# Optimization experiments

Measured on AMD Instinct MI355X. Metric: run time of the kernel, lower is better.

## Reference

```python
import jax, jax.numpy as jnp
import numpy as np

D_MODEL, D_STATE, D_CONV, EXPAND, HEADDIM, NGROUPS, CHUNK = 1024, 64, 4, 2, 64, 1, 64
D_INNER = EXPAND * D_MODEL          # 2048
NHEADS = D_INNER // HEADDIM         # 32
CONV_DIM = D_INNER + 2 * NGROUPS * D_STATE  # 2176
D_IN_PROJ = 2 * D_INNER + 2 * NGROUPS * D_STATE + NHEADS  # 4256
EPS = 1e-5


def segsum(x):
    """x: (..., T) -> (..., T, T) with out[i,j]=sum_{j<k<=i} x[k], -inf above diag."""
    T = x.shape[-1]
    i = jnp.arange(T)[:, None]
    j = jnp.arange(T)[None, :]
    xr = jnp.where(i > j, x[..., :, None], 0.0)   # keep x[...,i] at (i,j) when i>j
    s = jnp.cumsum(xr, axis=-2)
    return jnp.where(i >= j, s, -jnp.inf)


def setup_inputs() -> dict:
    key = jax.random.key(0)
    ks = jax.random.split(key, 10)
    B, L = 4, 4096
    u = jax.random.normal(ks[0], (B, L, D_MODEL), dtype=jnp.float32)
    in_proj_w = jax.random.normal(ks[1], (D_IN_PROJ, D_MODEL), dtype=jnp.float32) * (D_MODEL ** -0.5)
    conv_w = jax.random.normal(ks[2], (CONV_DIM, D_CONV), dtype=jnp.float32) * (D_CONV ** -0.5)
    conv_b = jax.random.normal(ks[3], (CONV_DIM,), dtype=jnp.float32) * 0.02
    init_states = jax.random.normal(ks[4], (NHEADS, HEADDIM, D_STATE), dtype=jnp.float32) * 0.02
    # dt_bias = inv softplus of dt sampled log-uniform in [1e-3, 1e-1]
    dt = jnp.exp(jax.random.uniform(ks[5], (NHEADS,)) * (np.log(0.1) - np.log(0.001)) + np.log(0.001))
    dt = jnp.clip(dt, 1e-4, None)
    dt_bias = dt + jnp.log(-jnp.expm1(-dt))
    A_log = jnp.log(jax.random.uniform(ks[6], (NHEADS,), minval=1.0, maxval=16.0))
    D = jnp.ones((NHEADS,), dtype=jnp.float32)
    norm_w = jnp.ones((D_INNER,), dtype=jnp.float32)
    out_proj_w = jax.random.normal(ks[7], (D_MODEL, D_INNER), dtype=jnp.float32) * (D_INNER ** -0.5)
    return {"u": u, "in_proj_w": in_proj_w, "conv_w": conv_w, "conv_b": conv_b,
            "init_states": init_states, "dt_bias": dt_bias, "A_log": A_log, "D": D,
            "norm_w": norm_w, "out_proj_w": out_proj_w}


def _forward(u, in_proj_w, conv_w, conv_b, init_states, dt_bias, A_log, D, norm_w, out_proj_w):
    b, L, _ = u.shape
    zxbcdt = jnp.einsum('bld,ed->ble', u, in_proj_w)
    z = zxbcdt[..., :D_INNER]
    xBC = zxbcdt[..., D_INNER:D_INNER + CONV_DIM]
    dt = jax.nn.softplus(zxbcdt[..., D_INNER + CONV_DIM:] + dt_bias)  # (b,L,h)
    # causal depthwise conv1d (padding=K-1, truncated to L) + SiLU
    xp = jnp.pad(xBC, ((0, 0), (D_CONV - 1, 0), (0, 0)))
    xBC = sum(xp[:, k:k + L, :] * conv_w[:, k] for k in range(D_CONV)) + conv_b
    xBC = jax.nn.silu(xBC)
    x = xBC[..., :D_INNER].reshape(b, L, NHEADS, HEADDIM)
    Bm = xBC[..., D_INNER:D_INNER + NGROUPS * D_STATE].reshape(b, L, NGROUPS, D_STATE)
    Cm = xBC[..., D_INNER + NGROUPS * D_STATE:].reshape(b, L, NGROUPS, D_STATE)
    A = -jnp.exp(A_log)  # (h,)
    # broadcast groups to heads (torch einsum broadcasts size-1 group dim)
    Bm = jnp.repeat(Bm, NHEADS // NGROUPS, axis=2)
    Cm = jnp.repeat(Cm, NHEADS // NGROUPS, axis=2)
    X = x * dt[..., None]          # (b,L,h,p)
    Adt = A * dt                   # (b,L,h)
    c = L // CHUNK
    Xc = X.reshape(b, c, CHUNK, NHEADS, HEADDIM)
    Bc = Bm.reshape(b, c, CHUNK, NHEADS, D_STATE)
    Cc = Cm.reshape(b, c, CHUNK, NHEADS, D_STATE)
    Ac = Adt.reshape(b, c, CHUNK, NHEADS).transpose(0, 3, 1, 2)  # (b,h,c,l)
    A_cumsum = jnp.cumsum(Ac, axis=-1)
    Lmat = jnp.exp(segsum(Ac))  # (b,h,c,l,l)
    Y_diag = jnp.einsum('bclhn,bcshn,bhcls,bcshp->bclhp', Cc, Bc, Lmat, Xc)
    decay_states = jnp.exp(A_cumsum[..., -1:] - A_cumsum)  # (b,h,c,l)
    states = jnp.einsum('bclhn,bhcl,bclhp->bchpn', Bc, decay_states, Xc)
    init = jnp.broadcast_to(init_states, (b,) + init_states.shape)[:, None]  # (b,1,h,p,n)
    states = jnp.concatenate([init, states], axis=1)  # (b,c+1,h,p,n)
    decay_chunk = jnp.exp(segsum(jnp.pad(A_cumsum[..., -1], ((0, 0), (0, 0), (1, 0)))))
    new_states = jnp.einsum('bhzc,bchpn->bzhpn', decay_chunk, states)
    states = new_states[:, :-1]
    state_decay_out = jnp.exp(A_cumsum)
    Y_off = jnp.einsum('bclhn,bchpn,bhcl->bclhp', Cc, states, state_decay_out)
    Y = (Y_diag + Y_off).reshape(b, L, NHEADS, HEADDIM) + x * D[:, None]
    y = Y.reshape(b, L, D_INNER)
    # gated RMSNorm (gate before norm)
    y = y * jax.nn.silu(z)
    y = y * jax.lax.rsqrt(jnp.mean(y * y, axis=-1, keepdims=True) + EPS) * norm_w
    return jnp.einsum('bld,ed->ble', y, out_proj_w)


def reference(u, in_proj_w, conv_w, conv_b, init_states, dt_bias, A_log, D, norm_w, out_proj_w):
    return _forward(u, in_proj_w, conv_w, conv_b, init_states, dt_bias, A_log, D, norm_w, out_proj_w)
```

## Files before the change

kernel.cpp:

```cpp
#include <hip/hip_runtime.h>
#include <math.h>

#define BATCH  4
#define LSEQ   4096
#define DMODEL 1024
#define DINNER 2048
#define NH     32
#define HD     64
#define DSTATE 64
#define CONVD  2176
#define NPROJ  4352
#define ZROW   4224
#define NCHUNK 64

typedef __attribute__((ext_vector_type(8))) short bf16x8;
typedef __attribute__((ext_vector_type(4))) float f32x4;

__device__ __forceinline__ float sigm(float x){ return 1.f/(1.f+expf(-x)); }

__device__ __forceinline__ unsigned short f2bf(float x){
    unsigned u = __float_as_uint(x);
    unsigned r = (u + 0x7fffu + ((u>>16)&1u)) >> 16;
    return (unsigned short)r;
}
__device__ __forceinline__ float bf2f(unsigned short h){
    return __uint_as_float(((unsigned)h)<<16);
}

__device__ __forceinline__ void gl2lds16(const unsigned short* g, short* l){
    __builtin_amdgcn_global_load_lds(
        (const __attribute__((address_space(1))) unsigned int*)g,
        (__attribute__((address_space(3))) unsigned int*)l, 16, 0, 0);
}

__global__ __launch_bounds__(256)
void f32_to_bf16(const float* __restrict__ in, unsigned short* __restrict__ o, size_t n)
{
    size_t i = ((size_t)blockIdx.x*256 + threadIdx.x)*8;
    if (i >= n) return;
    float4 a = *(const float4*)(in + i);
    float4 b = *(const float4*)(in + i + 4);
    uint4 v;
    v.x = (unsigned)f2bf(a.x) | ((unsigned)f2bf(a.y)<<16);
    v.y = (unsigned)f2bf(a.z) | ((unsigned)f2bf(a.w)<<16);
    v.z = (unsigned)f2bf(b.x) | ((unsigned)f2bf(b.y)<<16);
    v.w = (unsigned)f2bf(b.z) | ((unsigned)f2bf(b.w)<<16);
    *(uint4*)(o + i) = v;
}

template<int EPI>
__global__ __launch_bounds__(256)
void gemm_mfma(const unsigned short* __restrict__ A,
               const unsigned short* __restrict__ B,
               int K, int lda, int ldc, int ntiles, int Mrows,
               float* __restrict__ Cf,
               unsigned short* __restrict__ zxbc,
               float* __restrict__ dtout,
               const float* __restrict__ dt_bias,
               unsigned short* __restrict__ halo)
{
    __shared__ short As[128*64];
    __shared__ short Bs[128*64];
    const int tid  = threadIdx.x;
    const int wave = tid >> 6;
    const int lane = tid & 63;

    const int GM  = 16;
    const int pid = blockIdx.x;
    const int gsz = GM * ntiles;
    const int grp = pid / gsz;
    const int rem = pid - grp*gsz;
    const int bm  = (grp*GM + (rem & (GM-1))) * 128;
    const int bn  = (rem / GM) * 128;

    const int wr = (wave >> 1) * 64;
    const int wc = (wave & 1) * 64;
    const int quad = lane >> 4;
    const int l15  = lane & 15;

    f32x4 acc[4][4];
    #pragma unroll
    for (int i=0;i<4;i++)
        #pragma unroll
        for (int j=0;j<4;j++)
            acc[i][j] = (f32x4){0.f,0.f,0.f,0.f};

    const int srow8 = lane >> 3;
    const int scolx = ((lane & 7) ^ srow8) * 8;
    const int rsw   = (l15 & 7);

    for (int k0 = 0; k0 < K; k0 += 64){
        #pragma unroll
        for (int s=0; s<4; s++){
            int t = wave*4 + s;
            int r = t*8 + srow8;
            gl2lds16(A + (size_t)(bm + r)*lda + k0 + scolx, &As[t*512]);
            gl2lds16(B + (size_t)(bn + r)*K   + k0 + scolx, &Bs[t*512]);
        }
        __syncthreads();
        #pragma unroll
        for (int ks=0; ks<2; ks++){
            bf16x8 af[4], bg[4];
            #pragma unroll
            for (int i=0;i<4;i++)
                af[i] = *(const bf16x8*)&As[(wr + i*16 + l15)*64 + (((ks*4 + quad) ^ rsw)<<3)];
            #pragma unroll
            for (int j=0;j<4;j++)
                bg[j] = *(const bf16x8*)&Bs[(wc + j*16 + l15)*64 + (((ks*4 + quad) ^ rsw)<<3)];
            #pragma unroll
            for (int i=0;i<4;i++)
                #pragma unroll
                for (int j=0;j<4;j++)
                    acc[i][j] = __builtin_amdgcn_mfma_f32_16x16x32_bf16(af[i], bg[j], acc[i][j], 0,0,0);
        }
        __syncthreads();
    }

    if (EPI == 0){
        #pragma unroll
        for (int i=0;i<4;i++)
            #pragma unroll
            for (int j=0;j<4;j++){
                int col = bn + wc + j*16 + l15;
                #pragma unroll
                for (int r=0;r<4;r++){
                    int row = bm + wr + i*16 + quad*4 + r;
                    Cf[(size_t)row*ldc + col] = acc[i][j][r];
                }
            }
    } else {
        if (bn < DINNER){
            #pragma unroll
            for (int i=0;i<4;i++)
                #pragma unroll
                for (int r=0;r<4;r++){
                    int row = bm + wr + i*16 + quad*4 + r;
                    #pragma unroll
                    for (int j=0;j<4;j++){
                        int col = bn + wc + j*16 + l15;
                        zxbc[(size_t)row*ZROW + col] = f2bf(acc[i][j][r]);
                    }
                }
        } else if (bn < DINNER + CONVD){
            #pragma unroll
            for (int i=0;i<4;i++)
                #pragma unroll
                for (int r=0;r<4;r++){
                    int row = bm + wr + i*16 + quad*4 + r;
                    int rel = row & 63;
                    int seg = (row >> 6) + 1;
                    #pragma unroll
                    for (int j=0;j<4;j++){
                        int col = bn + wc + j*16 + l15;
                        unsigned short v = f2bf(acc[i][j][r]);
                        zxbc[(size_t)row*ZROW + col] = v;
                        if (rel >= 61 && seg*64 < Mrows)
                            halo[((size_t)(seg*3 + (rel-61)))*CONVD + (col - DINNER)] = v;
                    }
                }
        } else if (wc == 0){
            #pragma unroll
            for (int j=0;j<2;j++){
                int h = j*16 + l15;
                #pragma unroll
                for (int i=0;i<4;i++)
                    #pragma unroll
                    for (int r=0;r<4;r++){
                        int row = bm + wr + i*16 + quad*4 + r;
                        float t = acc[i][j][r] + dt_bias[h];
                        dtout[(size_t)row*NH + h] = (t > 20.f) ? t : log1pf(expf(t));
                    }
            }
        }
    }
}

__global__ __launch_bounds__(256)
void conv_inplace(unsigned short* __restrict__ zxbc,
                  const unsigned short* __restrict__ halo,
                  const float* __restrict__ conv_w, const float* __restrict__ conv_b)
{
    int c = blockIdx.x*256 + threadIdx.x;
    if (c >= CONVD) return;
    int seg = blockIdx.y;
    const float w0=conv_w[c*4+0], w1=conv_w[c*4+1], w2=conv_w[c*4+2], w3=conv_w[c*4+3];
    const float bias = conv_b[c];
    float x0=0.f, x1=0.f, x2=0.f;
    if ((seg & 63) != 0){
        const unsigned short* hp = halo + (size_t)(seg*3)*CONVD + c;
        x0 = bf2f(hp[0]); x1 = bf2f(hp[CONVD]); x2 = bf2f(hp[2*CONVD]);
    }
    unsigned short* p = zxbc + (size_t)(seg*64)*ZROW + DINNER + c;
    for (int i=0;i<64;i++){
        float x3 = bf2f(*p);
        float v = fmaf(w0,x0,fmaf(w1,x1,fmaf(w2,x2,fmaf(w3,x3,bias))));
        *p = f2bf(v * sigm(v));
        x0=x1; x1=x2; x2=x3; p += ZROW;
    }
}

__global__ __launch_bounds__(256)
void states_intra(const unsigned short* __restrict__ zxbc,
                  const float* __restrict__ dtbuf,
                  const float* __restrict__ A_log,
                  unsigned short* __restrict__ locst,
                  float* __restrict__ acsbuf,
                  float* __restrict__ csumbuf)
{
    const int h = blockIdx.x, c = blockIdx.y;
    __shared__ unsigned short XT[64*72];
    __shared__ unsigned short BT[64*72];
    __shared__ float dt_sh[64], acs_sh[64], w_sh[64];
    const int tid = threadIdx.x;
    const size_t row0 = (size_t)(c*64)*ZROW;

    if (tid < 64) dt_sh[tid] = dtbuf[(size_t)(c*64+tid)*NH + h];
    __syncthreads();
    if (tid == 0){
        float Ah = -expf(A_log[h]); float s = 0.f;
        for (int l=0;l<64;l++){ s = fmaf(Ah, dt_sh[l], s); acs_sh[l] = s; }
    }
    __syncthreads();
    const float a63 = acs_sh[63];
    if (tid < 64){
        float a = acs_sh[tid];
        acsbuf[((size_t)c*NH + h)*64 + tid] = a;
        w_sh[tid] = expf(a63 - a) * dt_sh[tid];
    }
    if (tid == 0) csumbuf[(size_t)c*NH + h] = a63;
    __syncthreads();

    {
        const int l  = tid >> 2;
        const int f4 = tid & 3;
        const unsigned short* xr = zxbc + row0 + (size_t)l*ZROW;
        const float w = w_sh[l];
        #pragma unroll
        for (int q=0;q<4;q++){
            int col = f4*4 + q*16;
            uint2 xv = *(const uint2*)(xr + DINNER + h*HD + col);
            uint2 bv = *(const uint2*)(xr + DINNER + DINNER + col);
            XT[(col+0)*72 + l] = (unsigned short)(xv.x & 0xffff);
            XT[(col+1)*72 + l] = (unsigned short)(xv.x >> 16);
            XT[(col+2)*72 + l] = (unsigned short)(xv.y & 0xffff);
            XT[(col+3)*72 + l] = (unsigned short)(xv.y >> 16);
            BT[(col+0)*72 + l] = f2bf(bf2f((unsigned short)(bv.x & 0xffff))*w);
            BT[(col+1)*72 + l] = f2bf(bf2f((unsigned short)(bv.x >> 16))*w);
            BT[(col+2)*72 + l] = f2bf(bf2f((unsigned short)(bv.y & 0xffff))*w);
            BT[(col+3)*72 + l] = f2bf(bf2f((unsigned short)(bv.y >> 16))*w);
        }
    }
    __syncthreads();

    const int wave = tid >> 6, lane = tid & 63;
    const int quad = lane >> 4, l15 = lane & 15;
    f32x4 acc[4];
    #pragma unroll
    for (int j=0;j<4;j++) acc[j] = (f32x4){0.f,0.f,0.f,0.f};
    #pragma unroll
    for (int ks=0;ks<2;ks++){
        bf16x8 af = *(const bf16x8*)&XT[(wave*16 + l15)*72 + ks*32 + quad*8];
        #pragma unroll
        for (int j=0;j<4;j++){
            bf16x8 bf = *(const bf16x8*)&BT[(j*16 + l15)*72 + ks*32 + quad*8];
            acc[j] = __builtin_amdgcn_mfma_f32_16x16x32_bf16(af, bf, acc[j], 0,0,0);
        }
    }
    const size_t sbase = ((size_t)c*NH + h)*4096;
    #pragma unroll
    for (int j=0;j<4;j++)
        #pragma unroll
        for (int r=0;r<4;r++){
            int p = wave*16 + quad*4 + r;
            int n = j*16 + l15;
            locst[sbase + (size_t)p*64 + n] = f2bf(acc[j][r]);
        }
}

__global__ __launch_bounds__(256)
void chunk_scan(unsigned short* __restrict__ states,
                const float* __restrict__ csumbuf,
                const float* __restrict__ init_states)
{
    const int h = blockIdx.x, half = blockIdx.y, b = blockIdx.z;
    __shared__ float cs_sh[64];
    const int tid = threadIdx.x;
    if (tid < 64) cs_sh[tid] = csumbuf[(size_t)(b*64 + tid)*NH + h];
    __syncthreads();
    const int e0 = half*2048 + tid*8;
    float S[8];
    {
        const float4* ip = (const float4*)(init_states + (size_t)h*4096 + e0);
        float4 v0 = ip[0], v1 = ip[1];
        S[0]=v0.x; S[1]=v0.y; S[2]=v0.z; S[3]=v0.w;
        S[4]=v1.x; S[5]=v1.y; S[6]=v1.z; S[7]=v1.w;
    }
    for (int zg=0; zg<8; zg++){
        uint4 L[8];
        #pragma unroll
        for (int k=0;k<8;k++)
            L[k] = *(const uint4*)(states + ((size_t)(b*64 + zg*8+k)*NH + h)*4096 + e0);
        #pragma unroll
        for (int k=0;k<8;k++){
            int z = zg*8 + k;
            float dec = expf(cs_sh[z]);
            uint4 o;
            o.x = (unsigned)f2bf(S[0]) | ((unsigned)f2bf(S[1])<<16);
            o.y = (unsigned)f2bf(S[2]) | ((unsigned)f2bf(S[3])<<16);
            o.z = (unsigned)f2bf(S[4]) | ((unsigned)f2bf(S[5])<<16);
            o.w = (unsigned)f2bf(S[6]) | ((unsigned)f2bf(S[7])<<16);
            *(uint4*)(states + ((size_t)(b*64 + z)*NH + h)*4096 + e0) = o;
            unsigned a[4] = {L[k].x, L[k].y, L[k].z, L[k].w};
            #pragma unroll
            for (int q=0;q<4;q++){
                float lo = bf2f((unsigned short)(a[q]&0xffff));
                float hi = bf2f((unsigned short)(a[q]>>16));
                S[q*2+0] = fmaf(dec, S[q*2+0], lo);
                S[q*2+1] = fmaf(dec, S[q*2+1], hi);
            }
        }
    }
}

__global__ __launch_bounds__(256)
void y_fused(unsigned short* __restrict__ zxbc,
             const float* __restrict__ dtbuf,
             const unsigned short* __restrict__ entst,
             const float* __restrict__ acsbuf,
             const float* __restrict__ Dvec)
{
    const int h = blockIdx.x, c = blockIdx.y;
    __shared__ unsigned short Cr[64*72];
    __shared__ unsigned short Ce[64*72];
    __shared__ unsigned short Bm[64*72];
    __shared__ unsigned short XT[64*72];
    __shared__ unsigned short Sv[64*72];
    __shared__ float acs_sh[64], dt_sh[64], ea_sh[64];
    const int tid = threadIdx.x;
    const size_t row0 = (size_t)(c*64)*ZROW;
    const size_t sbase = ((size_t)c*NH + h)*4096;

    if (tid < 64){
        float a = acsbuf[((size_t)c*NH + h)*64 + tid];
        acs_sh[tid] = a;
        ea_sh[tid]  = expf(a);
        dt_sh[tid]  = dtbuf[(size_t)(c*64 + tid)*NH + h];
    }
    __syncthreads();

    {
        const int l  = tid >> 2;
        const int f4 = tid & 3;
        const unsigned short* xr = zxbc + row0 + (size_t)l*ZROW;
        const float el = ea_sh[l];
        #pragma unroll
        for (int q=0;q<4;q++){
            int col = f4*4 + q*16;
            uint2 cv = *(const uint2*)(xr + DINNER + DINNER + DSTATE + col);
            uint2 bv = *(const uint2*)(xr + DINNER + DINNER + col);
            uint2 xv = *(const uint2*)(xr + DINNER + h*HD + col);
            *(uint2*)&Cr[l*72 + col] = cv;
            *(uint2*)&Bm[l*72 + col] = bv;
            unsigned short* ce = &Ce[l*72 + col];
            ce[0] = f2bf(bf2f((unsigned short)(cv.x & 0xffff))*el);
            ce[1] = f2bf(bf2f((unsigned short)(cv.x >> 16))*el);
            ce[2] = f2bf(bf2f((unsigned short)(cv.y & 0xffff))*el);
            ce[3] = f2bf(bf2f((unsigned short)(cv.y >> 16))*el);
            XT[(col+0)*72 + l] = (unsigned short)(xv.x & 0xffff);
            XT[(col+1)*72 + l] = (unsigned short)(xv.x >> 16);
            XT[(col+2)*72 + l] = (unsigned short)(xv.y & 0xffff);
            XT[(col+3)*72 + l] = (unsigned short)(xv.y >> 16);
            *(uint2*)&Sv[l*72 + col] = *(const uint2*)(entst + sbase + (size_t)l*64 + col);
        }
    }
    __syncthreads();

    const int wave = tid >> 6, lane = tid & 63;
    const int quad = lane >> 4, l15 = lane & 15;

    f32x4 g[4];
    #pragma unroll
    for (int j=0;j<4;j++) g[j] = (f32x4){0.f,0.f,0.f,0.f};
    #pragma unroll
    for (int ks=0;ks<2;ks++){
        bf16x8 af = *(const bf16x8*)&Cr[(wave*16 + l15)*72 + ks*32 + quad*8];
        #pragma unroll
        for (int j=0;j<4;j++){
            bf16x8 bf = *(const bf16x8*)&Bm[(j*16 + l15)*72 + ks*32 + quad*8];
            g[j] = __builtin_amdgcn_mfma_f32_16x16x32_bf16(af, bf, g[j], 0,0,0);
        }
    }
    __syncthreads();

    const float Dh = Dvec[h];
    #pragma unroll
    for (int j=0;j<4;j++)
        #pragma unroll
        for (int r=0;r<4;r++){
            int l = wave*16 + quad*4 + r;
            int s = j*16 + l15;
            float v = (s <= l) ? g[j][r]*expf(acs_sh[l]-acs_sh[s])*dt_sh[s] : 0.f;
            if (s == l) v += Dh;
            Bm[l*72 + s] = f2bf(v);
        }
    __syncthreads();

    f32x4 y[4];
    #pragma unroll
    for (int j=0;j<4;j++) y[j] = (f32x4){0.f,0.f,0.f,0.f};
    #pragma unroll
    for (int ks=0;ks<2;ks++){
        bf16x8 a1 = *(const bf16x8*)&Bm[(wave*16 + l15)*72 + ks*32 + quad*8];
        bf16x8 a2 = *(const bf16x8*)&Ce[(wave*16 + l15)*72 + ks*32 + quad*8];
        #pragma unroll
        for (int j=0;j<4;j++){
            bf16x8 b1 = *(const bf16x8*)&XT[(j*16 + l15)*72 + ks*32 + quad*8];
            bf16x8 b2 = *(const bf16x8*)&Sv[(j*16 + l15)*72 + ks*32 + quad*8];
            y[j] = __builtin_amdgcn_mfma_f32_16x16x32_bf16(a1, b1, y[j], 0,0,0);
            y[j] = __builtin_amdgcn_mfma_f32_16x16x32_bf16(a2, b2, y[j], 0,0,0);
        }
    }

    #pragma unroll
    for (int j=0;j<4;j++)
        #pragma unroll
        for (int r=0;r<4;r++){
            int l = wave*16 + quad*4 + r;
            int p = j*16 + l15;
            zxbc[row0 + (size_t)l*ZROW + DINNER + h*HD + p] = f2bf(y[j][r]);
        }
}

__global__ __launch_bounds__(256)
void gate_norm(unsigned short* __restrict__ zxbc, const float* __restrict__ norm_w)
{
    const int m = blockIdx.x;
    const int tid = threadIdx.x;
    unsigned short* row = zxbc + (size_t)m*ZROW;
    uint4 zv = *(const uint4*)(row + tid*8);
    uint4 yv = *(const uint4*)(row + DINNER + tid*8);
    unsigned zz[4] = {zv.x, zv.y, zv.z, zv.w};
    unsigned yy[4] = {yv.x, yv.y, yv.z, yv.w};
    float g[8];
    float acc = 0.f;
    #pragma unroll
    for (int q=0;q<4;q++){
        float zl = bf2f((unsigned short)(zz[q]&0xffff));
        float zh = bf2f((unsigned short)(zz[q]>>16));
        float yl = bf2f((unsigned short)(yy[q]&0xffff));
        float yh = bf2f((unsigned short)(yy[q]>>16));
        g[q*2+0] = yl * zl * sigm(zl);
        g[q*2+1] = yh * zh * sigm(zh);
        acc += g[q*2]*g[q*2] + g[q*2+1]*g[q*2+1];
    }
    #pragma unroll
    for (int o=32;o>0;o>>=1) acc += __shfl_down(acc, o, 64);
    __shared__ float red[4];
    if ((tid & 63)==0) red[tid>>6] = acc;
    __syncthreads();
    float tot = red[0]+red[1]+red[2]+red[3];
    float scale = rsqrtf(tot * (1.f/2048.f) + 1e-5f);
    const float* nw = norm_w + tid*8;
    float4 w0 = *(const float4*)nw;
    float4 w1 = *(const float4*)(nw+4);
    float Wv[8] = {w0.x,w0.y,w0.z,w0.w,w1.x,w1.y,w1.z,w1.w};
    uint4 ov;
    unsigned ow[4];
    #pragma unroll
    for (int q=0;q<4;q++){
        unsigned short lo = f2bf(g[q*2+0]*scale*Wv[q*2+0]);
        unsigned short hi = f2bf(g[q*2+1]*scale*Wv[q*2+1]);
        ow[q] = (unsigned)lo | ((unsigned)hi<<16);
    }
    ov.x=ow[0]; ov.y=ow[1]; ov.z=ow[2]; ov.w=ow[3];
    *(uint4*)(row + tid*8) = ov;
}

extern "C" void kernel_launch(void* const* d_in, const int* in_sizes, int n_in,
                              void* d_out, int out_size, void* d_ws, size_t ws_size,
                              hipStream_t stream) {
    const float* u           = (const float*)d_in[0];
    const float* in_proj_w   = (const float*)d_in[1];
    const float* conv_w      = (const float*)d_in[2];
    const float* conv_b      = (const float*)d_in[3];
    const float* init_states = (const float*)d_in[4];
    const float* dt_bias     = (const float*)d_in[5];
    const float* A_log       = (const float*)d_in[6];
    const float* Dv          = (const float*)d_in[7];
    const float* norm_w      = (const float*)d_in[8];
    const float* out_proj_w  = (const float*)d_in[9];
    float* out = (float*)d_out;
    char* wsb = (char*)d_ws;

    const size_t BIG_BYTES = 226197504;
    const bool big = (ws_size >= BIG_BYTES);
    const int nb = big ? BATCH : 1;
    const size_t Mrows = (size_t)nb * LSEQ;

    size_t off = 0;
    unsigned short* zxbc    = (unsigned short*)(wsb + off); off += Mrows*ZROW*2;
    unsigned short* statesz = (unsigned short*)(wsb + off);
    unsigned short* ubf     = statesz;
    off += Mrows/64 * NH*HD*DSTATE*2;
    unsigned short* wibf    = (unsigned short*)(wsb + off); off += (size_t)NPROJ*DMODEL*2;
    unsigned short* woutbf  = (unsigned short*)(wsb + off); off += (size_t)DMODEL*DINNER*2;
    float*          dtbuf   = (float*)(wsb + off);   off += Mrows*NH*4;
    float*          acsbuf  = (float*)(wsb + off);   off += Mrows/64 * NH*64*4;
    float*          csumbuf = (float*)(wsb + off);   off += Mrows/64 * NH*4;
    unsigned short* halo    = (unsigned short*)(wsb + off); off += Mrows/64 * 3*CONVD*2;

    f32_to_bf16<<<dim3((4256*1024/8 + 255)/256), 256, 0, stream>>>(
        in_proj_w, wibf, (size_t)4256*1024);
    f32_to_bf16<<<dim3(1024*2048/8/256), 256, 0, stream>>>(
        out_proj_w, woutbf, (size_t)1024*2048);

    const int npass = big ? 1 : BATCH;
    for (int b=0; b<npass; b++){
        const float* ub   = u   + (size_t)b*LSEQ*DMODEL;
        float*       outb = out + (size_t)b*LSEQ*DMODEL;
        const int mt = (int)(Mrows/128);

        f32_to_bf16<<<dim3(Mrows*DMODEL/8/256), 256, 0, stream>>>(
            ub, ubf, Mrows*DMODEL);
        gemm_mfma<1><<<dim3((NPROJ/128) * mt), 256, 0, stream>>>(
            ubf, wibf, DMODEL, DMODEL, 0, NPROJ/128, (int)Mrows,
            nullptr, zxbc, dtbuf, dt_bias, halo);
        conv_inplace<<<dim3(9, (unsigned)(Mrows/64)), 256, 0, stream>>>(
            zxbc, halo, conv_w, conv_b);
        states_intra<<<dim3(NH, (unsigned)(Mrows/64)), 256, 0, stream>>>(
            zxbc, dtbuf, A_log, statesz, acsbuf, csumbuf);
        chunk_scan<<<dim3(NH, 2, nb), 256, 0, stream>>>(
            statesz, csumbuf, init_states);
        y_fused<<<dim3(NH, (unsigned)(Mrows/64)), 256, 0, stream>>>(
            zxbc, dtbuf, statesz, acsbuf, Dv);
        gate_norm<<<dim3((unsigned)Mrows), 256, 0, stream>>>(zxbc, norm_w);
        gemm_mfma<0><<<dim3((DMODEL/128) * mt), 256, 0, stream>>>(
            zxbc, woutbf, DINNER, ZROW, DMODEL, DMODEL/128, (int)Mrows,
            outb, nullptr, nullptr, nullptr, nullptr);
    }
}
```

Baseline: 609.0 us.

## Double-buffer LDS tiles in MFMA GEMM to overlap loads with compute

Turns the GEMM's shared-memory A/B tiles into two ping-pong buffers. The next K-tile is prefetched with direct global-to-LDS loads while MFMAs run on the current tile, which hides global load latency. Row pointers are also precomputed outside the loop. LDS use per block doubles to 64 KB, which may lower occupancy, and the hunk shown does not make clear whether the barrier placement still gives correct synchronisation.

```diff
diff --git a/kernel.cpp b/kernel.cpp
--- a/kernel.cpp
+++ b/kernel.cpp
@@ -59,8 +59,8 @@
                const float* __restrict__ dt_bias,
                unsigned short* __restrict__ halo)
 {
-    __shared__ short As[128*64];
-    __shared__ short Bs[128*64];
+    __shared__ short As[2][128*64];
+    __shared__ short Bs[2][128*64];
     const int tid  = threadIdx.x;
     const int wave = tid >> 6;
     const int lane = tid & 63;
@@ -89,24 +89,42 @@
     const int scolx = ((lane & 7) ^ srow8) * 8;
     const int rsw   = (l15 & 7);
 
-    for (int k0 = 0; k0 < K; k0 += 64){
-        #pragma unroll
-        for (int s=0; s<4; s++){
-            int t = wave*4 + s;
-            int r = t*8 + srow8;
-            gl2lds16(A + (size_t)(bm + r)*lda + k0 + scolx, &As[t*512]);
-            gl2lds16(B + (size_t)(bn + r)*K   + k0 + scolx, &Bs[t*512]);
-        }
-        __syncthreads();
+    const unsigned short* pa = A + (size_t)(bm + srow8)*lda + scolx;
+    const unsigned short* pb = B + (size_t)(bn + srow8)*K   + scolx;
+
+    const int nkt = K >> 6;
+
+    #pragma unroll
+    for (int s=0; s<4; s++){
+        int t = wave*4 + s;
+        gl2lds16(pa + (size_t)(t*8)*lda, &As[0][t*512]);
+        gl2lds16(pb + (size_t)(t*8)*K,   &Bs[0][t*512]);
+    }
+    __syncthreads();
+
+    for (int kt = 0; kt < nkt; ++kt){
+        if (kt+1 < nkt){
+            const int nb_ = (kt+1) & 1;
+            const int ko  = (kt+1) << 6;
+            #pragma unroll
+            for (int s=0; s<4; s++){
+                int t = wave*4 + s;
+                gl2lds16(pa + (size_t)(t*8)*lda + ko, &As[nb_][t*512]);
+                gl2lds16(pb + (size_t)(t*8)*K   + ko, &Bs[nb_][t*512]);
+            }
+        }
+        const short* Asl = &As[kt & 1][0];
+        const short* Bsl = &Bs[kt & 1][0];
         #pragma unroll
         for (int ks=0; ks<2; ks++){
+            const int co = ((ks*4 + quad) ^ rsw) << 3;
             bf16x8 af[4], bg[4];
             #pragma unroll
             for (int i=0;i<4;i++)
-                af[i] = *(const bf16x8*)&As[(wr + i*16 + l15)*64 + (((ks*4 + quad) ^ rsw)<<3)];
+                af[i] = *(const bf16x8*)&Asl[(wr + i*16 + l15)*64 + co];
             #pragma unroll
             for (int j=0;j<4;j++)
-                bg[j] = *(const bf16x8*)&Bs[(wc + j*16 + l15)*64 + (((ks*4 + quad) ^ rsw)<<3)];
+                bg[j] = *(const bf16x8*)&Bsl[(wc + j*16 + l15)*64 + co];
             #pragma unroll
             for (int i=0;i<4;i++)
                 #pragma unroll
```

Result: faster. 584.9 us (-4.0%).

## Pre-swizzle weights into MFMA fragment layout and double-buffer A tiles in GEMM

Applied to the files above, without the earlier changes.

The weight conversion kernel now writes bf16 weights in an MFMA-fragment-ordered layout, so each GEMM wave can load its B operands straight from global memory into registers instead of staging them through LDS. The A tile staging is double-buffered in LDS, with the next k-tile's A and B loads issued while the current one is computed. This is meant to halve LDS traffic and hide global load latency behind compute. In exchange it raises register pressure (two sets of eight B fragments held per wave), and the padded weight rows (4256 up to 4352) depend on the fragment kernel covering only 266 row-groups.

```diff
diff --git a/kernel.cpp b/kernel.cpp
--- a/kernel.cpp
+++ b/kernel.cpp
@@ -48,10 +48,56 @@
     *(uint4*)(o + i) = v;
 }
 
+__global__ __launch_bounds__(256)
+void f32_to_bf16_frag(const float* __restrict__ in, unsigned short* __restrict__ o,
+                      int K, size_t total)
+{
+    size_t tid = (size_t)blockIdx.x*256 + threadIdx.x;
+    if (tid >= total) return;
+    const int lane = (int)(tid & 63);
+    const size_t rem = tid >> 6;
+    const int nk32 = K >> 5;
+    const int k32  = (int)(rem % nk32);
+    const size_t n16 = rem / nk32;
+    const float* s = in + (n16*16 + (size_t)(lane & 15))*K + k32*32 + (lane >> 4)*8;
+    float4 a = *(const float4*)s;
+    float4 b = *(const float4*)(s + 4);
+    uint4 v;
+    v.x = (unsigned)f2bf(a.x) | ((unsigned)f2bf(a.y)<<16);
+    v.y = (unsigned)f2bf(a.z) | ((unsigned)f2bf(a.w)<<16);
+    v.z = (unsigned)f2bf(b.x) | ((unsigned)f2bf(b.y)<<16);
+    v.w = (unsigned)f2bf(b.z) | ((unsigned)f2bf(b.w)<<16);
+    *(uint4*)(o + tid*8) = v;
+}
+
+#define STAGEA(ktl) { \
+    const int nb_ = (ktl) & 1; const int ko_ = (ktl) << 6; \
+    _Pragma("unroll") for (int s=0; s<4; s++){ \
+        int t_ = wave*4 + s; \
+        gl2lds16(pa + (size_t)(t_*8)*lda + ko_, &As[nb_][t_*512]); \
+    } }
+
+#define LOADBG(dst, ktl) { \
+    const unsigned short* fb_ = bbase + (size_t)(ktl)*1024; \
+    _Pragma("unroll") for (int ks=0; ks<2; ks++) \
+    _Pragma("unroll") for (int j=0; j<4; j++) \
+        dst[ks*4+j] = *(const bf16x8*)(fb_ + ((size_t)j*nk32 + ks)*512); }
+
+#define COMPUTE(Asl, bg) { \
+    _Pragma("unroll") for (int ks=0; ks<2; ks++){ \
+        const int co_ = ((ks*4 + quad) ^ rsw) << 3; \
+        bf16x8 af[4]; \
+        _Pragma("unroll") for (int i=0;i<4;i++) \
+            af[i] = *(const bf16x8*)&(Asl)[(wr + i*16 + l15)*64 + co_]; \
+        _Pragma("unroll") for (int i=0;i<4;i++) \
+        _Pragma("unroll") for (int j=0;j<4;j++) \
+            acc[i][j] = __builtin_amdgcn_mfma_f32_16x16x32_bf16(af[i], bg[ks*4+j], acc[i][j], 0,0,0); \
+    } }
+
 template<int EPI>
 __global__ __launch_bounds__(256)
 void gemm_mfma(const unsigned short* __restrict__ A,
-               const unsigned short* __restrict__ B,
+               const unsigned short* __restrict__ Bf,
                int K, int lda, int ldc, int ntiles, int Mrows,
                float* __restrict__ Cf,
                unsigned short* __restrict__ zxbc,
@@ -59,8 +105,7 @@
                const float* __restrict__ dt_bias,
                unsigned short* __restrict__ halo)
 {
-    __shared__ short As[128*64];
-    __shared__ short Bs[128*64];
+    __shared__ short As[2][128*64];
     const int tid  = threadIdx.x;
     const int wave = tid >> 6;
     const int lane = tid & 63;
@@ -89,30 +134,29 @@
     const int scolx = ((lane & 7) ^ srow8) * 8;
     const int rsw   = (l15 & 7);
 
-    for (int k0 = 0; k0 < K; k0 += 64){
-        #pragma unroll
-        for (int s=0; s<4; s++){
-            int t = wave*4 + s;
-            int r = t*8 + srow8;
-            gl2lds16(A + (size_t)(bm + r)*lda + k0 + scolx, &As[t*512]);
-            gl2lds16(B + (size_t)(bn + r)*K   + k0 + scolx, &Bs[t*512]);
-        }
+    const unsigned short* pa = A + (size_t)(bm + srow8)*lda + scolx;
+
+    const int nk32 = K >> 5;
+    const unsigned short* bbase = Bf + ((size_t)((bn + wc) >> 4) * nk32) * 512 + lane*8;
+
+    const int nkt = K >> 6;
+
+    bf16x8 bgA[8], bgB[8];
+
+    STAGEA(0);
+    LOADBG(bgA, 0);
+    __syncthreads();
+
+    for (int kt = 0; kt < nkt; kt += 2){
+        STAGEA(kt+1);
+        LOADBG(bgB, kt+1);
+        COMPUTE(As[0], bgA);
         __syncthreads();
-        #pragma unroll
-        for (int ks=0; ks<2; ks++){
-            bf16x8 af[4], bg[4];
-            #pragma unroll
-            for (int i=0;i<4;i++)
-                af[i] = *(const bf16x8*)&As[(wr + i*16 + l15)*64 + (((ks*4 + quad) ^ rsw)<<3)];
-            #pragma unroll
-            for (int j=0;j<4;j++)
-                bg[j] = *(const bf16x8*)&Bs[(wc + j*16 + l15)*64 + (((ks*4 + quad) ^ rsw)<<3)];
-            #pragma unroll
-            for (int i=0;i<4;i++)
-                #pragma unroll
-                for (int j=0;j<4;j++)
-                    acc[i][j] = __builtin_amdgcn_mfma_f32_16x16x32_bf16(af[i], bg[j], acc[i][j], 0,0,0);
-        }
+        if (kt+2 < nkt){
+            STAGEA(kt+2);
+            LOADBG(bgA, kt+2);
+        }
+        COMPUTE(As[1], bgB);
         __syncthreads();
     }
 
@@ -509,10 +553,10 @@
     float*          csumbuf = (float*)(wsb + off);   off += Mrows/64 * NH*4;
     unsigned short* halo    = (unsigned short*)(wsb + off); off += Mrows/64 * 3*CONVD*2;
 
-    f32_to_bf16<<<dim3((4256*1024/8 + 255)/256), 256, 0, stream>>>(
-        in_proj_w, wibf, (size_t)4256*1024);
-    f32_to_bf16<<<dim3(1024*2048/8/256), 256, 0, stream>>>(
-        out_proj_w, woutbf, (size_t)1024*2048);
+    f32_to_bf16_frag<<<dim3(2128), 256, 0, stream>>>(
+        in_proj_w, wibf, DMODEL, (size_t)266*32*64);
+    f32_to_bf16_frag<<<dim3(1024), 256, 0, stream>>>(
+        out_proj_w, woutbf, DINNER, (size_t)64*64*64);
 
     const int npass = big ? 1 : BATCH;
     for (int b=0; b<npass; b++){
```

New measurement: 597.3 us. Within noise of the previous version (-1.9%).
